# Performance work log

Measured on AMD Instinct MI355X. Metric: run time of the kernel, lower is better.

The kernel has to match this reference:

```python
import jax, jax.numpy as jnp
import numpy as np

B_SZ, C_IN, C_OUT, H, W = 16, 32, 32, 128, 128
K, CODE, PAD, FACTOR = 3, 2, 1, 1.0

def setup_inputs() -> dict:
    key = jax.random.key(0)
    ks = jax.random.split(key, 7)
    s = 0.05
    return {
        "x": jax.random.normal(ks[0], (B_SZ, C_IN, H, W), jnp.float32),
        "codes": jax.random.normal(ks[1], (B_SZ, CODE, CODE), jnp.float32),
        "weight": jax.random.normal(ks[2], (C_OUT, C_IN, K, K), jnp.float32) * s,
        "A": jax.random.normal(ks[3], (C_IN, CODE, K, K), jnp.float32) * s,
        "Bm": jax.random.normal(ks[4], (C_OUT, CODE, K, K), jnp.float32) * s,
        "bias": jax.random.normal(ks[5], (C_OUT,), jnp.float32) * s,
        "bias_context": jax.random.normal(ks[6], (CODE, C_OUT), jnp.float32) * s,
    }

def reference(x, codes, weight, A, Bm, bias, bias_context):
    # hypernetwork weight synthesis: [b, out, in, k, k]
    w_ctx = jnp.einsum('ickl,bcr->birkl', A, codes)            # [b, in, code, k, k]
    w_ctx = jnp.einsum('birkl,orkl->boikl', w_ctx, Bm)         # [b, out, in, k, k]
    combined_weight = weight[None] + FACTOR * w_ctx
    # per-sample bias from diagonal of codes
    diag = jnp.diagonal(codes, axis1=-2, axis2=-1)             # [b, code]
    combined_bias = bias[None] + FACTOR * (diag @ bias_context)  # [b, out]
    # circular padding then per-sample VALID conv (== unfold + einsum)
    xp = jnp.pad(x, ((0, 0), (0, 0), (PAD, PAD), (PAD, PAD)), mode='wrap')
    def conv_one(xi, wi):
        return jax.lax.conv_general_dilated(
            xi[None], wi, window_strides=(1, 1), padding='VALID',
            dimension_numbers=('NCHW', 'OIHW', 'NCHW'))[0]
    out = jax.vmap(conv_one)(xp, combined_weight)              # [b, out, H, W]
    return out + combined_bias[:, :, None, None]
```

## Files before the change

### kernel.cpp

```cpp
#include <hip/hip_runtime.h>

typedef short bf16x8 __attribute__((ext_vector_type(8)));
typedef float f32x4  __attribute__((ext_vector_type(4)));
typedef unsigned int u32;

#define HH 128
#define WW 128

__device__ __forceinline__ u32 cvt_pk_bf16(float lo, float hi) {
    u32 r;
    asm volatile("v_cvt_pk_bf16_f32 %0, %1, %2" : "=v"(r) : "v"(lo), "v"(hi));
    return r;
}

__device__ __forceinline__ void lds_barrier() {
    asm volatile("s_waitcnt lgkmcnt(0)" ::: "memory");
    __builtin_amdgcn_s_barrier();
    __builtin_amdgcn_sched_barrier(0);
}

__global__ __launch_bounds__(1024, 1) void geps_mfma_kernel(
    const float* __restrict__ x, const float* __restrict__ codes,
    const float* __restrict__ weight, const float* __restrict__ A,
    const float* __restrict__ Bm, const float* __restrict__ bias,
    const float* __restrict__ bctx, float* __restrict__ out)
{
    __shared__ bf16x8 lds_x[5120];
    __shared__ bf16x8 lds_w[1152];
    __shared__ float  lds_ctx[576];
    __shared__ float  lds_b[32];

    const int tid  = threadIdx.x;
    const int l    = tid & 63;
    const int wvid = tid >> 6;
    const int row4 = wvid >> 2;
    const int nq   = wvid & 3;

    const int orig = blockIdx.x;
    const int vb   = (orig & 7) * 32 + (orig >> 3);
    const int b    = vb >> 4;
    const int grp  = vb & 15;
    const int h0   = grp * 8;

    float2 f[5][4];
    #pragma unroll
    for (int it = 0; it < 5; ++it) {
        int idx = it * 1024 + tid;
        int cp = idx & 63, jh = (idx >> 6) & 1, ig = (idx >> 7) & 3, rr = idx >> 9;
        int grow = (h0 - 1 + rr) & 127;
        const float* src =
            x + ((size_t)(b * 32 + ig * 8 + jh * 4) * HH + grow) * WW + cp * 2;
        #pragma unroll
        for (int jj = 0; jj < 4; ++jj)
            f[it][jj] = *(const float2*)(src + (size_t)jj * HH * WW);
    }

    const float c00 = codes[b * 4 + 0];
    const float c01 = codes[b * 4 + 1];
    const float c10 = codes[b * 4 + 2];
    const float c11 = codes[b * 4 + 3];
    if (tid < 576) {
        int j = tid;
        int i = j / 18, rem = j % 18, r = rem / 9, kl = rem % 9;
        float a0 = A[(i * 2 + 0) * 9 + kl];
        float a1 = A[(i * 2 + 1) * 9 + kl];
        lds_ctx[j] = (r == 0) ? (a0 * c00 + a1 * c10) : (a0 * c01 + a1 * c11);
    }
    if (tid < 32) lds_b[tid] = bias[tid] + c00 * bctx[tid] + c11 * bctx[32 + tid];
    lds_barrier();

    for (int j = tid; j < 1152; j += 1024) {
        int kl = j >> 7, rem = j & 127, o = rem >> 2, kb = rem & 3;
        float m0 = Bm[(o * 2 + 0) * 9 + kl];
        float m1 = Bm[(o * 2 + 1) * 9 + kl];
        float wf[8];
        #pragma unroll
        for (int jj = 0; jj < 8; ++jj) {
            int i = kb * 8 + jj;
            wf[jj] = weight[(o * 32 + i) * 9 + kl]
                   + lds_ctx[i * 18 + kl] * m0
                   + lds_ctx[i * 18 + 9 + kl] * m1;
        }
        u32 pk[4];
        #pragma unroll
        for (int q = 0; q < 4; ++q) pk[q] = cvt_pk_bf16(wf[2 * q], wf[2 * q + 1]);
        *(uint4*)&lds_w[kl * 128 + (o >> 4) * 64 + kb * 16 + (o & 15)] =
            make_uint4(pk[0], pk[1], pk[2], pk[3]);
    }

    #pragma unroll
    for (int it = 0; it < 5; ++it) {
        int idx = it * 1024 + tid;
        int cp = idx & 63, jh = (idx >> 6) & 1, ig = (idx >> 7) & 3, rr = idx >> 9;
        int c0 = cp * 2;
        u32 a0 = cvt_pk_bf16(f[it][0].x, f[it][1].x);
        u32 a1 = cvt_pk_bf16(f[it][2].x, f[it][3].x);
        u32 b0 = cvt_pk_bf16(f[it][0].y, f[it][1].y);
        u32 b1 = cvt_pk_bf16(f[it][2].y, f[it][3].y);
        int didx = (c0 >> 4) * 64 + ig * 16 + (c0 & 15);
        *(uint2*)((char*)lds_x + rr * 8192 + didx * 16 + jh * 8) =
            make_uint2(a0, a1);
        *(uint2*)((char*)lds_x + rr * 8192 + (didx + 1) * 16 + jh * 8) =
            make_uint2(b0, b1);
    }
    lds_barrier();

    const int awb = (l >> 4) * 16 + (l & 15);
    bf16x8 af[9][2];
    #pragma unroll
    for (int kl = 0; kl < 9; ++kl)
        #pragma unroll
        for (int oh = 0; oh < 2; ++oh)
            af[kl][oh] = lds_w[kl * 128 + oh * 64 + awb];

    const int p = l & 15, igf = l >> 4;
    int bb[3];
    #pragma unroll
    for (int dl = -1; dl <= 1; ++dl) {
        int pq = p + dl;
        bb[dl + 1] = (pq & 15) + ((pq >> 4) << 6) + igf * 16;
    }

    float blr[2][4];
    #pragma unroll
    for (int oh = 0; oh < 2; ++oh)
        #pragma unroll
        for (int r = 0; r < 4; ++r)
            blr[oh][r] = lds_b[oh * 16 + (l >> 4) * 4 + r];

    #pragma unroll
    for (int c = 0; c < 2; ++c) {
        f32x4 acc[2][2];
        #pragma unroll
        for (int oh = 0; oh < 2; ++oh)
            #pragma unroll
            for (int q = 0; q < 2; ++q) acc[oh][q] = (f32x4){0.f, 0.f, 0.f, 0.f};

        #pragma unroll
        for (int lc = 0; lc < 3; ++lc) {
            #pragma unroll
            for (int k = 0; k < 3; ++k) {
                const bf16x8 a0 = af[k * 3 + lc][0];
                const bf16x8 a1 = af[k * 3 + lc][1];
                const int s = 4 * c + row4 + k;
                #pragma unroll
                for (int q = 0; q < 2; ++q) {
                    int t = (bb[lc] + (nq * 2 + q) * 64) & 511;
                    bf16x8 bfv = lds_x[s * 512 + t];
                    acc[0][q] = __builtin_amdgcn_mfma_f32_16x16x32_bf16(
                        a0, bfv, acc[0][q], 0, 0, 0);
                    acc[1][q] = __builtin_amdgcn_mfma_f32_16x16x32_bf16(
                        a1, bfv, acc[1][q], 0, 0, 0);
                }
            }
        }

        float* bounce = (float*)((char*)lds_x + 4 * c * 8192);
        #pragma unroll
        for (int oh = 0; oh < 2; ++oh) {
            lds_barrier();
            #pragma unroll
            for (int q = 0; q < 2; ++q)
                #pragma unroll
                for (int r = 0; r < 4; ++r) {
                    int o16  = (l >> 4) * 4 + r;
                    int col  = (nq * 2 + q) * 16 + (l & 15);
                    int col2 = (col + o16 * 4) & 127;
                    bounce[(o16 * 4 + row4) * 128 + col2] =
                        acc[oh][q][r] + blr[oh][r];
                }
            lds_barrier();
            const int ch = oh * 16 + wvid;
            #pragma unroll
            for (int k2 = 0; k2 < 2; ++k2) {
                int hrow = 2 * k2 + (l >> 5);
                int lcol = (l & 31) * 4;
                int pcol = (lcol + wvid * 4) & 127;
                f32x4 v = *(const f32x4*)&bounce[(wvid * 4 + hrow) * 128 + pcol];
                __builtin_nontemporal_store(
                    v, (f32x4*)&out[((size_t)(b * 32 + ch) * HH +
                                     (h0 + 4 * c + hrow)) * WW + lcol]);
            }
        }
        if (c == 0) lds_barrier();
    }
}

extern "C" void kernel_launch(void* const* d_in, const int* in_sizes, int n_in,
                              void* d_out, int out_size, void* d_ws, size_t ws_size,
                              hipStream_t stream) {
    const float* x      = (const float*)d_in[0];
    const float* codes  = (const float*)d_in[1];
    const float* weight = (const float*)d_in[2];
    const float* A      = (const float*)d_in[3];
    const float* Bm     = (const float*)d_in[4];
    const float* bias   = (const float*)d_in[5];
    const float* bctx   = (const float*)d_in[6];
    float* out = (float*)d_out;

    hipLaunchKernelGGL(geps_mfma_kernel, dim3(256), dim3(1024), 0, stream,
                       x, codes, weight, A, Bm, bias, bctx, out);
}
```

Measured before the change: 21.29 us.

## Split halo input loads to overlap with first-half MFMA and fold weight synthesis into registers

The input tile load is split in two. Only the six rows needed for the first half of the output are loaded before the first barrier. The remaining rows are issued as global loads that stay in flight during the first MFMA pass, and are written to LDS after it. Weight synthesis now computes the A·codes context per thread in registers instead of staging it through LDS, which removes one block-wide barrier and its dependent LDS round trip. The second-half A fragments are re-read from LDS per MFMA to cut register pressure, at the cost of extra LDS reads in the inner loop.

```diff
diff --git a/kernel.cpp b/kernel.cpp
--- a/kernel.cpp
+++ b/kernel.cpp
@@ -27,7 +27,6 @@
 {
     __shared__ bf16x8 lds_x[5120];
     __shared__ bf16x8 lds_w[1152];
-    __shared__ float  lds_ctx[576];
     __shared__ float  lds_b[32];
 
     const int tid  = threadIdx.x;
@@ -42,9 +41,42 @@
     const int grp  = vb & 15;
     const int h0   = grp * 8;
 
-    float2 f[5][4];
-    #pragma unroll
-    for (int it = 0; it < 5; ++it) {
+    const float c00 = codes[b * 4 + 0];
+    const float c01 = codes[b * 4 + 1];
+    const float c10 = codes[b * 4 + 2];
+    const float c11 = codes[b * 4 + 3];
+    float bv = 0.f, bx0 = 0.f, bx1 = 0.f;
+    if (tid < 32) { bv = bias[tid]; bx0 = bctx[tid]; bx1 = bctx[32 + tid]; }
+
+    const int j0 = tid, j1 = tid + 1024;
+    const int kl0 = j0 >> 7, o0 = (j0 & 127) >> 2, kb0 = j0 & 3;
+    float m0a, m1a, wga[8], a0a[8], a1a[8];
+    m0a = Bm[(o0 * 2 + 0) * 9 + kl0];
+    m1a = Bm[(o0 * 2 + 1) * 9 + kl0];
+    #pragma unroll
+    for (int jj = 0; jj < 8; ++jj) {
+        int i = kb0 * 8 + jj;
+        wga[jj] = weight[(o0 * 32 + i) * 9 + kl0];
+        a0a[jj] = A[(i * 2 + 0) * 9 + kl0];
+        a1a[jj] = A[(i * 2 + 1) * 9 + kl0];
+    }
+    const int kl1 = j1 >> 7, o1 = (j1 & 127) >> 2, kb1 = j1 & 3;
+    float m0b = 0, m1b = 0, wgb[8], a0b[8], a1b[8];
+    if (tid < 128) {
+        m0b = Bm[(o1 * 2 + 0) * 9 + kl1];
+        m1b = Bm[(o1 * 2 + 1) * 9 + kl1];
+        #pragma unroll
+        for (int jj = 0; jj < 8; ++jj) {
+            int i = kb1 * 8 + jj;
+            wgb[jj] = weight[(o1 * 32 + i) * 9 + kl1];
+            a0b[jj] = A[(i * 2 + 0) * 9 + kl1];
+            a1b[jj] = A[(i * 2 + 1) * 9 + kl1];
+        }
+    }
+
+    float2 f[3][4];
+    #pragma unroll
+    for (int it = 0; it < 3; ++it) {
         int idx = it * 1024 + tid;
         int cp = idx & 63, jh = (idx >> 6) & 1, ig = (idx >> 7) & 3, rr = idx >> 9;
         int grow = (h0 - 1 + rr) & 127;
@@ -55,41 +87,38 @@
             f[it][jj] = *(const float2*)(src + (size_t)jj * HH * WW);
     }
 
-    const float c00 = codes[b * 4 + 0];
-    const float c01 = codes[b * 4 + 1];
-    const float c10 = codes[b * 4 + 2];
-    const float c11 = codes[b * 4 + 3];
-    if (tid < 576) {
-        int j = tid;
-        int i = j / 18, rem = j % 18, r = rem / 9, kl = rem % 9;
-        float a0 = A[(i * 2 + 0) * 9 + kl];
-        float a1 = A[(i * 2 + 1) * 9 + kl];
-        lds_ctx[j] = (r == 0) ? (a0 * c00 + a1 * c10) : (a0 * c01 + a1 * c11);
-    }
-    if (tid < 32) lds_b[tid] = bias[tid] + c00 * bctx[tid] + c11 * bctx[32 + tid];
-    lds_barrier();
-
-    for (int j = tid; j < 1152; j += 1024) {
-        int kl = j >> 7, rem = j & 127, o = rem >> 2, kb = rem & 3;
-        float m0 = Bm[(o * 2 + 0) * 9 + kl];
-        float m1 = Bm[(o * 2 + 1) * 9 + kl];
+    {
         float wf[8];
         #pragma unroll
         for (int jj = 0; jj < 8; ++jj) {
-            int i = kb * 8 + jj;
-            wf[jj] = weight[(o * 32 + i) * 9 + kl]
-                   + lds_ctx[i * 18 + kl] * m0
-                   + lds_ctx[i * 18 + 9 + kl] * m1;
+            float t0 = a0a[jj] * c00 + a1a[jj] * c10;
+            float t1 = a0a[jj] * c01 + a1a[jj] * c11;
+            wf[jj] = wga[jj] + t0 * m0a + t1 * m1a;
         }
         u32 pk[4];
         #pragma unroll
         for (int q = 0; q < 4; ++q) pk[q] = cvt_pk_bf16(wf[2 * q], wf[2 * q + 1]);
-        *(uint4*)&lds_w[kl * 128 + (o >> 4) * 64 + kb * 16 + (o & 15)] =
+        *(uint4*)&lds_w[kl0 * 128 + (o0 >> 4) * 64 + kb0 * 16 + (o0 & 15)] =
             make_uint4(pk[0], pk[1], pk[2], pk[3]);
     }
-
-    #pragma unroll
-    for (int it = 0; it < 5; ++it) {
+    if (tid < 128) {
+        float wf[8];
+        #pragma unroll
+        for (int jj = 0; jj < 8; ++jj) {
+            float t0 = a0b[jj] * c00 + a1b[jj] * c10;
+            float t1 = a0b[jj] * c01 + a1b[jj] * c11;
+            wf[jj] = wgb[jj] + t0 * m0b + t1 * m1b;
+        }
+        u32 pk[4];
+        #pragma unroll
+        for (int q = 0; q < 4; ++q) pk[q] = cvt_pk_bf16(wf[2 * q], wf[2 * q + 1]);
+        *(uint4*)&lds_w[kl1 * 128 + (o1 >> 4) * 64 + kb1 * 16 + (o1 & 15)] =
+            make_uint4(pk[0], pk[1], pk[2], pk[3]);
+    }
+    if (tid < 32) lds_b[tid] = bv + c00 * bx0 + c11 * bx1;
+
+    #pragma unroll
+    for (int it = 0; it < 3; ++it) {
         int idx = it * 1024 + tid;
         int cp = idx & 63, jh = (idx >> 6) & 1, ig = (idx >> 7) & 3, rr = idx >> 9;
         int c0 = cp * 2;
@@ -103,15 +132,28 @@
         *(uint2*)((char*)lds_x + rr * 8192 + (didx + 1) * 16 + jh * 8) =
             make_uint2(b0, b1);
     }
+
+    float2 fd[2][4];
+    #pragma unroll
+    for (int it = 0; it < 2; ++it) {
+        int idx = it * 1024 + tid;
+        int cp = idx & 63, jh = (idx >> 6) & 1, ig = (idx >> 7) & 3;
+        int rr = 6 + (idx >> 9);
+        int grow = (h0 - 1 + rr) & 127;
+        const float* src =
+            x + ((size_t)(b * 32 + ig * 8 + jh * 4) * HH + grow) * WW + cp * 2;
+        #pragma unroll
+        for (int jj = 0; jj < 4; ++jj)
+            fd[it][jj] = *(const float2*)(src + (size_t)jj * HH * WW);
+    }
+
     lds_barrier();
 
     const int awb = (l >> 4) * 16 + (l & 15);
-    bf16x8 af[9][2];
+    bf16x8 af0[9];
     #pragma unroll
     for (int kl = 0; kl < 9; ++kl)
-        #pragma unroll
-        for (int oh = 0; oh < 2; ++oh)
-            af[kl][oh] = lds_w[kl * 128 + oh * 64 + awb];
+        af0[kl] = lds_w[kl * 128 + awb];
 
     const int p = l & 15, igf = l >> 4;
     int bb[3];
@@ -128,34 +170,50 @@
         for (int r = 0; r < 4; ++r)
             blr[oh][r] = lds_b[oh * 16 + (l >> 4) * 4 + r];
 
-    #pragma unroll
-    for (int c = 0; c < 2; ++c) {
-        f32x4 acc[2][2];
-        #pragma unroll
-        for (int oh = 0; oh < 2; ++oh)
-            #pragma unroll
-            for (int q = 0; q < 2; ++q) acc[oh][q] = (f32x4){0.f, 0.f, 0.f, 0.f};
-
-        #pragma unroll
-        for (int lc = 0; lc < 3; ++lc) {
-            #pragma unroll
-            for (int k = 0; k < 3; ++k) {
-                const bf16x8 a0 = af[k * 3 + lc][0];
-                const bf16x8 a1 = af[k * 3 + lc][1];
-                const int s = 4 * c + row4 + k;
-                #pragma unroll
-                for (int q = 0; q < 2; ++q) {
-                    int t = (bb[lc] + (nq * 2 + q) * 64) & 511;
-                    bf16x8 bfv = lds_x[s * 512 + t];
-                    acc[0][q] = __builtin_amdgcn_mfma_f32_16x16x32_bf16(
-                        a0, bfv, acc[0][q], 0, 0, 0);
-                    acc[1][q] = __builtin_amdgcn_mfma_f32_16x16x32_bf16(
-                        a1, bfv, acc[1][q], 0, 0, 0);
-                }
+    f32x4 acc[2][2];
+    #pragma unroll
+    for (int oh = 0; oh < 2; ++oh)
+        #pragma unroll
+        for (int q = 0; q < 2; ++q) acc[oh][q] = (f32x4){0.f, 0.f, 0.f, 0.f};
+
+    #pragma unroll
+    for (int lc = 0; lc < 3; ++lc) {
+        #pragma unroll
+        for (int k = 0; k < 3; ++k) {
+            const bf16x8 a0 = af0[k * 3 + lc];
+            const bf16x8 a1 = lds_w[(k * 3 + lc) * 128 + 64 + awb];
+            const int s = row4 + k;
+            #pragma unroll
+            for (int q = 0; q < 2; ++q) {
+                int t = (bb[lc] + (nq * 2 + q) * 64) & 511;
+                bf16x8 bfv = lds_x[s * 512 + t];
+                acc[0][q] = __builtin_amdgcn_mfma_f32_16x16x32_bf16(
+                    a0, bfv, acc[0][q], 0, 0, 0);
+                acc[1][q] = __builtin_amdgcn_mfma_f32_16x16x32_bf16(
+                    a1, bfv, acc[1][q], 0, 0, 0);
             }
         }
-
-        float* bounce = (float*)((char*)lds_x + 4 * c * 8192);
+    }
+
+    #pragma unroll
+    for (int it = 0; it < 2; ++it) {
+        int idx = it * 1024 + tid;
+        int cp = idx & 63, jh = (idx >> 6) & 1, ig = (idx >> 7) & 3;
+        int rr = 6 + (idx >> 9);
+        int c0 = cp * 2;
+        u32 a0 = cvt_pk_bf16(fd[it][0].x, fd[it][1].x);
+        u32 a1 = cvt_pk_bf16(fd[it][2].x, fd[it][3].x);
+        u32 b0 = cvt_pk_bf16(fd[it][0].y, fd[it][1].y);
+        u32 b1 = cvt_pk_bf16(fd[it][2].y, fd[it][3].y);
+        int didx = (c0 >> 4) * 64 + ig * 16 + (c0 & 15);
+        *(uint2*)((char*)lds_x + rr * 8192 + didx * 16 + jh * 8) =
+            make_uint2(a0, a1);
+        *(uint2*)((char*)lds_x + rr * 8192 + (didx + 1) * 16 + jh * 8) =
+            make_uint2(b0, b1);
+    }
+
+    {
+        float* bounce = (float*)lds_x;
         #pragma unroll
         for (int oh = 0; oh < 2; ++oh) {
             lds_barrier();
@@ -178,11 +236,64 @@
                 int pcol = (lcol + wvid * 4) & 127;
                 f32x4 v = *(const f32x4*)&bounce[(wvid * 4 + hrow) * 128 + pcol];
                 __builtin_nontemporal_store(
+                    v, (f32x4*)&out[((size_t)(b * 32 + ch) * HH + (h0 + hrow)) *
+                                    WW + lcol]);
+            }
+        }
+    }
+
+    #pragma unroll
+    for (int oh = 0; oh < 2; ++oh)
+        #pragma unroll
+        for (int q = 0; q < 2; ++q) acc[oh][q] = (f32x4){0.f, 0.f, 0.f, 0.f};
+
+    #pragma unroll
+    for (int lc = 0; lc < 3; ++lc) {
+        #pragma unroll
+        for (int k = 0; k < 3; ++k) {
+            const bf16x8 a0 = af0[k * 3 + lc];
+            const bf16x8 a1 = lds_w[(k * 3 + lc) * 128 + 64 + awb];
+            const int s = 4 + row4 + k;
+            #pragma unroll
+            for (int q = 0; q < 2; ++q) {
+                int t = (bb[lc] + (nq * 2 + q) * 64) & 511;
+                bf16x8 bfv = lds_x[s * 512 + t];
+                acc[0][q] = __builtin_amdgcn_mfma_f32_16x16x32_bf16(
+                    a0, bfv, acc[0][q], 0, 0, 0);
+                acc[1][q] = __builtin_amdgcn_mfma_f32_16x16x32_bf16(
+                    a1, bfv, acc[1][q], 0, 0, 0);
+            }
+        }
+    }
+
+    {
+        float* bounce = (float*)((char*)lds_x + 4 * 8192);
+        #pragma unroll
+        for (int oh = 0; oh < 2; ++oh) {
+            lds_barrier();
+            #pragma unroll
+            for (int q = 0; q < 2; ++q)
+                #pragma unroll
+                for (int r = 0; r < 4; ++r) {
+                    int o16  = (l >> 4) * 4 + r;
+                    int col  = (nq * 2 + q) * 16 + (l & 15);
+                    int col2 = (col + o16 * 4) & 127;
+                    bounce[(o16 * 4 + row4) * 128 + col2] =
+                        acc[oh][q][r] + blr[oh][r];
+                }
+            lds_barrier();
+            const int ch = oh * 16 + wvid;
+            #pragma unroll
+            for (int k2 = 0; k2 < 2; ++k2) {
+                int hrow = 2 * k2 + (l >> 5);
+                int lcol = (l & 31) * 4;
+                int pcol = (lcol + wvid * 4) & 127;
+                f32x4 v = *(const f32x4*)&bounce[(wvid * 4 + hrow) * 128 + pcol];
+                __builtin_nontemporal_store(
                     v, (f32x4*)&out[((size_t)(b * 32 + ch) * HH +
-                                     (h0 + 4 * c + hrow)) * WW + lcol]);
+                                     (h0 + 4 + hrow)) * WW + lcol]);
             }
         }
-        if (c == 0) lds_barrier();
     }
 }
 
```

After: 23.55 us. 10.6% more time.
